# Performance work log

Measured on AMD Instinct MI355X. Metric: run time of the kernel, lower is better.

## Reference

```python
import jax, jax.numpy as jnp
import numpy as np

B, S, H, K, HOP = 32, 512, 768, 4, 3


def setup_inputs() -> dict:
    key = jax.random.key(0)
    ks = jax.random.split(key, 18)
    sc = 0.02
    n = lambda k, shp: (jax.random.normal(k, shp, dtype=jnp.float32) * sc)
    inp = {
        "question": jax.random.normal(ks[0], (B, H), dtype=jnp.float32),
        "text": jax.random.normal(ks[1], (B, S, H), dtype=jnp.float32),
        # per-head MultiheadAttention params (stored as [in,out], i.e. W.T of torch Linear)
        "pw_W": n(ks[2], (K, H, H)), "pw_b": n(ks[3], (K, H)),
        "Ws_W": n(ks[4], (K, H, H)), "Ws_b": n(ks[5], (K, H)),
        "Wt_W": n(ks[6], (K, H, H)), "Wt_b": n(ks[7], (K, H)),
        "We_W": n(ks[8], (K, H)), "We_b": n(ks[9], (K,)),
        # head_weight: Linear(K -> 1)
        "headw_W": n(ks[10], (K,)), "headw_b": n(ks[11], (1,)),
        # GRUCell(input=2H, hidden=H); stored as [in, 3H] (r,z,n order as torch)
        "gru_Wih": n(ks[12], (2 * H, 3 * H)), "gru_Whh": n(ks[13], (H, 3 * H)),
        "gru_bih": n(ks[14], (3 * H,)), "gru_bhh": n(ks[15], (3 * H,)),
        "is_training": 0,
    }
    return inp


def _gru_cell(x, h, Wih, Whh, bih, bhh):
    gx = x @ Wih + bih            # [B,3H]
    gh = h @ Whh + bhh            # [B,3H]
    xr, xz, xn = jnp.split(gx, 3, axis=-1)
    hr, hz, hn = jnp.split(gh, 3, axis=-1)
    r = jax.nn.sigmoid(xr + hr)
    z = jax.nn.sigmoid(xz + hz)
    n = jnp.tanh(xn + r * hn)
    return (1.0 - z) * n + z * h


def reference(question, text, pw_W, pw_b, Ws_W, Ws_b, Wt_W, Wt_b, We_W, We_b,
              headw_W, headw_b, gru_Wih, gru_Whh, gru_bih, gru_bhh, is_training):
    # Dropout layers act as identity (eval mode).
    batch_idx = jnp.arange(text.shape[0])
    # text projection + W_s(text) are question-independent -> hoist out of hop loop
    text_p = jnp.einsum('bsh,khj->kbsj', text, pw_W) + pw_b[:, None, None, :]   # [K,B,S,H]
    W_hs = jnp.einsum('kbsh,khj->kbsj', text_p, Ws_W) + Ws_b[:, None, None, :]  # [K,B,S,H]

    h = jnp.zeros((text.shape[0], H), dtype=question.dtype)
    h_states = []
    predict_prob = None
    for hop in range(HOP):
        W_ht = jnp.einsum('bh,khj->kbj', question, Wt_W) + Wt_b[:, None, :]     # [K,B,H]
        scores = jnp.einsum('kbsh,kh->kbs', jnp.tanh(W_hs + W_ht[:, :, None, :]), We_W) \
                 + We_b[:, None, None]                                          # [K,B,S]
        alpha = jax.nn.softmax(scores, axis=2)                                  # softmax over S
        alpha_linear = jnp.einsum('kbs,k->bs', alpha, headw_W) + headw_b        # [B,S]
        scale = jnp.sqrt(jnp.sum(alpha_linear ** 2, axis=1, keepdims=True))
        prob = alpha_linear / scale
        if hop == 0:
            predict_prob = prob
        idx = jnp.argmax(alpha_linear, axis=1)                                  # [B]
        max_text = text[batch_idx, idx]                                         # [B,H]
        x = jnp.concatenate([question, max_text], axis=1)                       # [B,2H]
        h = _gru_cell(x, h, gru_Wih, gru_Whh, gru_bih, gru_bhh)
        h_states.append(h)
        question = h
    return predict_prob, jnp.stack(h_states, axis=1)                            # [B,S],[B,HOP,H]
```

## Files before the change

kernel.cpp:

```cpp
#include <hip/hip_runtime.h>

typedef unsigned short u16;
typedef __bf16 bf16x8 __attribute__((ext_vector_type(8)));
typedef float f32x4 __attribute__((ext_vector_type(4)));

#define NB 32
#define NS 512
#define NH 768
#define NK 4
#define NBS 16384
#define H3 2304
#define HH 589824

__device__ inline float bf2f(u16 u) {
    unsigned x = ((unsigned)u) << 16;
    return __builtin_bit_cast(float, x);
}
__device__ inline u16 f2bf(float f) {
    unsigned u = __builtin_bit_cast(unsigned, f);
    u += 0x7fffu + ((u >> 16) & 1u);
    return (u16)(u >> 16);
}
__device__ inline float tanh_fast(float x) {
    float e = __expf(2.f * x);
    return 1.f - 2.f * __builtin_amdgcn_rcpf(e + 1.f);
}
__device__ inline float sig_fast(float x) {
    return __builtin_amdgcn_rcpf(1.f + __expf(-x));
}
__device__ inline void gld16(const u16* g, u16* l) {
    __builtin_amdgcn_global_load_lds(
        (const __attribute__((address_space(1))) unsigned int*)g,
        (__attribute__((address_space(3))) unsigned int*)l, 16, 0, 0);
}


__global__ void prep_kernel(const float* __restrict__ WsW, const float* __restrict__ pwb,
                            const float* __restrict__ Wsb, float* __restrict__ combB,
                            const float* __restrict__ question,
                            float* __restrict__ q_f32, float* __restrict__ hT,
                            float* __restrict__ sx, float* __restrict__ sh,
                            const float* __restrict__ Web, float* __restrict__ scores,
                            const float* __restrict__ pwW,
                            u16* __restrict__ WsTH, u16* __restrict__ WsTL,
                            u16* __restrict__ pwH, u16* __restrict__ pwL,
                            const float* __restrict__ text, u16* __restrict__ textH,
                            int tier, int splitText)
{
    int bid = blockIdx.x, t = threadIdx.x;
    if (bid < 48) {
        int idx = bid * 64 + (t >> 2);
        int ph = t & 3;
        int k = idx / NH, j = idx % NH;
        const float* W = WsW + (long)k * HH + j;
        const float* pb = pwb + k * NH;
        float acc = 0.f;
        #pragma unroll 8
        for (int m = ph * 192; m < ph * 192 + 192; ++m)
            acc += pb[m] * W[(long)m * NH];
        acc += __shfl_xor(acc, 1);
        acc += __shfl_xor(acc, 2);
        if (ph == 0) combB[idx] = acc + Wsb[idx];
    } else if (bid < 144) {
        int idx = (bid - 48) * 256 + t;
        q_f32[idx] = question[idx];
    } else if (bid < 240) {
        int idx = (bid - 144) * 256 + t;
        hT[idx] = 0.f;
    } else if (bid < 816) {
        int idx = (bid - 240) * 256 + t;
        if (idx < 73728) sx[idx] = 0.f;
        else sh[idx - 73728] = 0.f;
    } else if (bid < 1072) {
        int idx = (bid - 816) * 256 + t;
        scores[idx] = Web[idx >> 14];
    } else if (bid < 3376) {
        if (tier < 2) return;
        __shared__ float tile[32][33];
        int bid2 = bid - 1072;
        int k = bid2 / 576, rem = bid2 % 576, tr = rem / 24, tc = rem % 24;
        const float* src = WsW + (long)k * HH;
        long dbase = (long)k * HH;
        int tx = t & 31, ty = t >> 5;
        #pragma unroll
        for (int i = 0; i < 4; ++i)
            tile[tx][ty + i*8] = src[(long)(tr*32 + ty + i*8) * NH + tc*32 + tx];
        __syncthreads();
        #pragma unroll
        for (int i = 0; i < 4; ++i) {
            float v = tile[ty + i*8][tx];
            u16 hv = f2bf(v);
            u16 lv = f2bf(v - bf2f(hv));
            long o = dbase + (long)(tc*32 + ty + i*8) * NH + tr*32 + tx;
            WsTH[o] = hv; WsTL[o] = lv;
        }
    } else if (bid < 5680) {
        if (tier < 2) return;
        long base = (long)(bid - 3376) * 1024 + t * 4;
        float4 v = *(const float4*)(pwW + base);
        ushort4 hv, lv;
        hv.x = f2bf(v.x); lv.x = f2bf(v.x - bf2f(hv.x));
        hv.y = f2bf(v.y); lv.y = f2bf(v.y - bf2f(hv.y));
        hv.z = f2bf(v.z); lv.z = f2bf(v.z - bf2f(hv.z));
        hv.w = f2bf(v.w); lv.w = f2bf(v.w - bf2f(hv.w));
        *(ushort4*)(pwH + base) = hv;
        *(ushort4*)(pwL + base) = lv;
    } else {
        if (!splitText) return;
        long base = (long)(bid - 5680) * 1024 + t * 4;
        float4 v = *(const float4*)(text + base);
        ushort4 hv;
        hv.x = f2bf(v.x);
        hv.y = f2bf(v.y);
        hv.z = f2bf(v.z);
        hv.w = f2bf(v.w);
        *(ushort4*)(textH + base) = hv;
    }
}

__global__ __launch_bounds__(256) void comb_mfma_kernel(
    const u16* __restrict__ WsTH, const u16* __restrict__ WsTL,
    const u16* __restrict__ pwH, const u16* __restrict__ pwL,
    u16* __restrict__ combTH, u16* __restrict__ combTL)
{
    __shared__ __align__(16) u16 AsH[128 * 32];
    __shared__ __align__(16) u16 AsL[128 * 32];
    __shared__ __align__(16) u16 BsH[128 * 32];
    __shared__ __align__(16) u16 BsL[128 * 32];
    const int t = threadIdx.x;
    const int wave = t >> 6, lane = t & 63;
    const int k = blockIdx.z;
    const long m0 = (long)blockIdx.x * 128;
    const int n0 = blockIdx.y * 128;
    const u16* AH = WsTH + (long)k * HH;
    const u16* AL = WsTL + (long)k * HH;
    const u16* BH = pwH + (long)k * HH;
    const u16* BL = pwL + (long)k * HH;

    const int r = t >> 2, ch = t & 3;
    const int wm = (wave & 1) * 64, wn = (wave >> 1) * 64;
    const int fr = lane & 15, fq = lane >> 4;

    f32x4 acc[4][4];
    #pragma unroll
    for (int i = 0; i < 4; ++i)
        #pragma unroll
        for (int j = 0; j < 4; ++j) acc[i][j] = (f32x4){0.f, 0.f, 0.f, 0.f};

    for (int k0 = 0; k0 < NH; k0 += 32) {
        gld16(AH + (m0 + r)      * NH + k0 + ch*8, AsH + t*8);
        gld16(AH + (m0 + 64 + r) * NH + k0 + ch*8, AsH + 2048 + t*8);
        gld16(AL + (m0 + r)      * NH + k0 + ch*8, AsL + t*8);
        gld16(AL + (m0 + 64 + r) * NH + k0 + ch*8, AsL + 2048 + t*8);
        gld16(BH + (long)(n0 + r)      * NH + k0 + ch*8, BsH + t*8);
        gld16(BH + (long)(n0 + 64 + r) * NH + k0 + ch*8, BsH + 2048 + t*8);
        gld16(BL + (long)(n0 + r)      * NH + k0 + ch*8, BsL + t*8);
        gld16(BL + (long)(n0 + 64 + r) * NH + k0 + ch*8, BsL + 2048 + t*8);
        __syncthreads();
        bf16x8 afH[4], afL[4], bfH[4], bfL[4];
        #pragma unroll
        for (int i = 0; i < 4; ++i) {
            afH[i] = *(const bf16x8*)(AsH + (wm + i*16 + fr)*32 + fq*8);
            afL[i] = *(const bf16x8*)(AsL + (wm + i*16 + fr)*32 + fq*8);
            bfH[i] = *(const bf16x8*)(BsH + (wn + i*16 + fr)*32 + fq*8);
            bfL[i] = *(const bf16x8*)(BsL + (wn + i*16 + fr)*32 + fq*8);
        }
        #pragma unroll
        for (int i = 0; i < 4; ++i)
            #pragma unroll
            for (int j = 0; j < 4; ++j) {
                acc[i][j] = __builtin_amdgcn_mfma_f32_16x16x32_bf16(afH[i], bfH[j], acc[i][j], 0, 0, 0);
                acc[i][j] = __builtin_amdgcn_mfma_f32_16x16x32_bf16(afH[i], bfL[j], acc[i][j], 0, 0, 0);
                acc[i][j] = __builtin_amdgcn_mfma_f32_16x16x32_bf16(afL[i], bfH[j], acc[i][j], 0, 0, 0);
            }
        __syncthreads();
    }
    long kb = (long)k * HH;
    #pragma unroll
    for (int i = 0; i < 4; ++i) {
        long m = m0 + wm + i*16 + fq*4;
        #pragma unroll
        for (int j = 0; j < 4; ++j) {
            long n = n0 + wn + j*16 + fr;
            #pragma unroll
            for (int rr = 0; rr < 4; ++rr) {
                float v = acc[i][j][rr];
                u16 hv = f2bf(v);
                u16 lv = f2bf(v - bf2f(hv));
                combTH[kb + (m + rr) * NH + n] = hv;
                combTL[kb + (m + rr) * NH + n] = lv;
            }
        }
    }
}

__global__ __launch_bounds__(256) void comb_valu_kernel(
    const float* __restrict__ pwW, const float* __restrict__ WsW,
    float* __restrict__ comb)
{
    __shared__ float AtT[32][68];
    __shared__ float Bt[32][132];
    const int t = threadIdx.x;
    const int m0 = blockIdx.x * 64, j0 = blockIdx.y * 128, k = blockIdx.z;
    const float* A = pwW + (long)k * HH;
    const float* B = WsW + (long)k * HH;
    const int r4 = (t >> 4) * 4, c8 = (t & 15) * 8;
    float acc[4][8];
    #pragma unroll
    for (int rr = 0; rr < 4; ++rr)
        #pragma unroll
        for (int cc = 0; cc < 8; ++cc) acc[rr][cc] = 0.f;
    for (int h0 = 0; h0 < NH; h0 += 32) {
        #pragma unroll
        for (int p = 0; p < 8; ++p) {
            int idx = p * 256 + t;
            int r = idx >> 5, hh = idx & 31;
            AtT[hh][r] = A[(long)(m0 + r) * NH + h0 + hh];
        }
        #pragma unroll
        for (int p = 0; p < 16; ++p) {
            int idx = p * 256 + t;
            int hh = idx >> 7, c = idx & 127;
            Bt[hh][c] = B[(long)(h0 + hh) * NH + j0 + c];
        }
        __syncthreads();
        for (int hh = 0; hh < 32; ++hh) {
            float4 av  = *(const float4*)&AtT[hh][r4];
            float4 bv0 = *(const float4*)&Bt[hh][c8];
            float4 bv1 = *(const float4*)&Bt[hh][c8 + 4];
            float a[4] = {av.x, av.y, av.z, av.w};
            float bb[8] = {bv0.x, bv0.y, bv0.z, bv0.w, bv1.x, bv1.y, bv1.z, bv1.w};
            #pragma unroll
            for (int rr = 0; rr < 4; ++rr)
                #pragma unroll
                for (int cc = 0; cc < 8; ++cc) acc[rr][cc] += a[rr] * bb[cc];
        }
        __syncthreads();
    }
    float* C = comb + (long)k * HH;
    #pragma unroll
    for (int rr = 0; rr < 4; ++rr)
        #pragma unroll
        for (int cc = 0; cc < 8; ++cc)
            C[(long)(m0 + r4 + rr) * NH + j0 + c8 + cc] = acc[rr][cc];
}

__global__ void split_combT_kernel(const float* __restrict__ comb,
                                   u16* __restrict__ combTH, u16* __restrict__ combTL)
{
    __shared__ float tile[32][33];
    int bid = blockIdx.x, t = threadIdx.x;
    int k = bid / 576, rem = bid % 576, tr = rem / 24, tc = rem % 24;
    const float* src = comb + (long)k * HH;
    long dbase = (long)k * HH;
    int tx = t & 31, ty = t >> 5;
    #pragma unroll
    for (int i = 0; i < 4; ++i)
        tile[tx][ty + i*8] = src[(long)(tr*32 + ty + i*8) * NH + tc*32 + tx];
    __syncthreads();
    #pragma unroll
    for (int i = 0; i < 4; ++i) {
        float v = tile[ty + i*8][tx];
        u16 hv = f2bf(v);
        u16 lv = f2bf(v - bf2f(hv));
        long o = dbase + (long)(tc*32 + ty + i*8) * NH + tr*32 + tx;
        combTH[o] = hv; combTL[o] = lv;
    }
}

template <int AM>
__global__ __launch_bounds__(256) void tp_gemm_kernel(
    const float* __restrict__ textf, const u16* __restrict__ textH,
    const u16* __restrict__ combTH, const u16* __restrict__ combTL,
    u16* __restrict__ TP)
{
    __shared__ __align__(16) u16 AsH[128 * 64];
    __shared__ __align__(16) u16 BsH[128 * 64];
    __shared__ __align__(16) u16 BsL[128 * 64];
    const int t = threadIdx.x;
    const int wave = t >> 6, lane = t & 63;
    const int k = blockIdx.z;
    const long m0 = (long)blockIdx.x * 128;
    const int n0 = blockIdx.y * 128;
    const u16* BH = combTH + (long)k * HH;
    const u16* BL = combTL + (long)k * HH;

    const int r = t >> 3, ch = t & 7;
    const int wm = (wave & 1) * 64, wn = (wave >> 1) * 64;
    const int fr = lane & 15, fq = lane >> 4;

    f32x4 acc[4][4];
    #pragma unroll
    for (int i = 0; i < 4; ++i)
        #pragma unroll
        for (int j = 0; j < 4; ++j) acc[i][j] = (f32x4){0.f, 0.f, 0.f, 0.f};

    for (int h0 = 0; h0 < NH; h0 += 64) {
        if (AM) {
            #pragma unroll
            for (int q = 0; q < 4; ++q)
                gld16(textH + (m0 + q*32 + r) * NH + h0 + ch*8, AsH + q*2048 + t*8);
        } else {
            #pragma unroll
            for (int p = 0; p < 8; ++p) {
                int task = p * 256 + t;
                int row = task >> 4, g = task & 15;
                float4 v = *(const float4*)(textf + (m0 + row) * NH + h0 + g*4);
                ushort4 hv;
                hv.x = f2bf(v.x);
                hv.y = f2bf(v.y);
                hv.z = f2bf(v.z);
                hv.w = f2bf(v.w);
                *(ushort4*)(AsH + row * 64 + g*4) = hv;
            }
        }
        #pragma unroll
        for (int q = 0; q < 4; ++q) {
            gld16(BH + (long)(n0 + q*32 + r) * NH + h0 + ch*8, BsH + q*2048 + t*8);
            gld16(BL + (long)(n0 + q*32 + r) * NH + h0 + ch*8, BsL + q*2048 + t*8);
        }
        __syncthreads();
        #pragma unroll
        for (int ks = 0; ks < 2; ++ks) {
            bf16x8 afH[4], bfH[4], bfL[4];
            #pragma unroll
            for (int i = 0; i < 4; ++i) {
                afH[i] = *(const bf16x8*)(AsH + (wm + i*16 + fr)*64 + ks*32 + fq*8);
                bfH[i] = *(const bf16x8*)(BsH + (wn + i*16 + fr)*64 + ks*32 + fq*8);
                bfL[i] = *(const bf16x8*)(BsL + (wn + i*16 + fr)*64 + ks*32 + fq*8);
            }
            #pragma unroll
            for (int i = 0; i < 4; ++i)
                #pragma unroll
                for (int j = 0; j < 4; ++j) {
                    acc[i][j] = __builtin_amdgcn_mfma_f32_16x16x32_bf16(afH[i], bfH[j], acc[i][j], 0, 0, 0);
                    acc[i][j] = __builtin_amdgcn_mfma_f32_16x16x32_bf16(afH[i], bfL[j], acc[i][j], 0, 0, 0);
                }
        }
        __syncthreads();
    }
    u16* out = TP + ((long)k * NBS + m0) * NH + n0;
    #pragma unroll
    for (int i = 0; i < 4; ++i) {
        #pragma unroll
        for (int rr = 0; rr < 4; ++rr) {
            int m = wm + i*16 + fq*4 + rr;
            #pragma unroll
            for (int j = 0; j < 4; ++j) {
                int n = wn + j*16 + fr;
                out[(long)m * NH + n] = f2bf(acc[i][j][rr]);
            }
        }
    }
}

__global__ __launch_bounds__(256) void score_pass_kernel(
    const u16* __restrict__ TP, const float* __restrict__ W_ht,
    const float* __restrict__ WeW, const float* __restrict__ Web,
    float* __restrict__ scores)
{
    __shared__ __align__(16) float bias_s[NH];
    __shared__ __align__(16) float we_s[NH];
    const int t = threadIdx.x;
    const int k = blockIdx.z, b = blockIdx.y;
    const int s0 = blockIdx.x * 32;
    for (int i = t; i < NH; i += 256) {
        bias_s[i] = W_ht[((k << 5) + b) * NH + i];
        we_s[i]   = WeW[k * NH + i];
    }
    __syncthreads();
    const int wave = t >> 6, lane = t & 63;
    const u16* tpb = TP + ((long)k * NBS + (b << 9) + s0) * NH;
    const float web = Web[k];
    for (int sr = wave; sr < 32; sr += 4) {
        const u16* row = tpb + (long)sr * NH;
        float part = 0.f;
        #pragma unroll
        for (int p = 0; p < 3; ++p) {
            const int j = p * 256 + lane * 4;
            ushort4 v = *(const ushort4*)(row + j);
            float4 bb = *(const float4*)(bias_s + j);
            float4 ww = *(const float4*)(we_s + j);
            part += tanh_fast(bf2f(v.x) + bb.x) * ww.x;
            part += tanh_fast(bf2f(v.y) + bb.y) * ww.y;
            part += tanh_fast(bf2f(v.z) + bb.z) * ww.z;
            part += tanh_fast(bf2f(v.w) + bb.w) * ww.w;
        }
        part += __shfl_xor(part, 1);
        part += __shfl_xor(part, 2);
        part += __shfl_xor(part, 4);
        part += __shfl_xor(part, 8);
        part += __shfl_xor(part, 16);
        part += __shfl_xor(part, 32);
        if (lane == 0) scores[(((k << 5) + b) << 9) + s0 + sr] = part + web;
    }
}

__global__ void init_scores_kernel(const float* __restrict__ Web,
                                   float* __restrict__ scores, int koff)
{
    int idx = (koff << 14) + blockIdx.x * 256 + threadIdx.x;
    scores[idx] = Web[idx >> 14];
}

__global__ __launch_bounds__(256) void wht2_kernel(
    const float* __restrict__ q, const float* __restrict__ WtW,
    const float* __restrict__ combB, const float* __restrict__ Wtb,
    float* __restrict__ W_ht)
{
    int bid = blockIdx.x;
    int k = bid / 96, rem = bid % 96, b = rem / 3, jt = rem % 3;
    int j = jt * 256 + threadIdx.x;
    const float* W = WtW + (long)k * HH + j;
    const float* qb = q + b * NH;
    float acc = 0.f;
    #pragma unroll 8
    for (int h = 0; h < NH; ++h) acc += qb[h] * W[(long)h * NH];
    W_ht[(k*NB + b) * NH + j] = acc + Wtb[k * NH + j] + combB[k * NH + j];
}

template <int AM>
__global__ __launch_bounds__(256) void fused_scores_mfma(
    const float* __restrict__ textf,
    const u16* __restrict__ textH, const u16* __restrict__ textL,
    const u16* __restrict__ combTH, const u16* __restrict__ combTL,
    const float* __restrict__ W_ht,
    const float* __restrict__ WeW, float* __restrict__ scores, int koff)
{
    __shared__ __align__(16) u16 AsH[128 * 32];
    __shared__ __align__(16) u16 AsL[128 * 32];
    __shared__ __align__(16) u16 BsH[128 * 32];
    __shared__ __align__(16) u16 BsL[128 * 32];
    __shared__ float wht_s[128];
    __shared__ float we_s[128];
    __shared__ float sred[128];
    const int t = threadIdx.x;
    const int wave = t >> 6, lane = t & 63;
    const int k = koff + blockIdx.z;
    const long m0 = (long)blockIdx.x * 128;
    const int n0 = blockIdx.y * 128;
    const int b = (int)(m0 >> 9), srow = (int)(m0 & 511);
    const u16* BH = combTH + (long)k * HH;
    const u16* BL = combTL + (long)k * HH;

    if (t < 128) {
        wht_s[t] = W_ht[((k << 5) + b) * NH + n0 + t];
        we_s[t]  = WeW[k * NH + n0 + t];
        sred[t]  = 0.f;
    }

    const int r = t >> 2, ch = t & 3;
    const int wm = (wave & 1) * 64, wn = (wave >> 1) * 64;
    const int fr = lane & 15, fq = lane >> 4;

    f32x4 acc[4][4];
    #pragma unroll
    for (int i = 0; i < 4; ++i)
        #pragma unroll
        for (int j = 0; j < 4; ++j) acc[i][j] = (f32x4){0.f, 0.f, 0.f, 0.f};

    for (int h0 = 0; h0 < NH; h0 += 32) {
        if (AM) {
            gld16(textH + (m0 + r)      * NH + h0 + ch*8, AsH + t*8);
            gld16(textH + (m0 + 64 + r) * NH + h0 + ch*8, AsH + 2048 + t*8);
            gld16(textL + (m0 + r)      * NH + h0 + ch*8, AsL + t*8);
            gld16(textL + (m0 + 64 + r) * NH + h0 + ch*8, AsL + 2048 + t*8);
        } else {
            #pragma unroll
            for (int p = 0; p < 4; ++p) {
                int task = p * 256 + t;
                int row = task >> 3, g = task & 7;
                float4 v = *(const float4*)(textf + (m0 + row) * NH + h0 + g*4);
                ushort4 hv, lv;
                hv.x = f2bf(v.x); lv.x = f2bf(v.x - bf2f(hv.x));
                hv.y = f2bf(v.y); lv.y = f2bf(v.y - bf2f(hv.y));
                hv.z = f2bf(v.z); lv.z = f2bf(v.z - bf2f(hv.z));
                hv.w = f2bf(v.w); lv.w = f2bf(v.w - bf2f(hv.w));
                *(ushort4*)(AsH + row * 32 + g*4) = hv;
                *(ushort4*)(AsL + row * 32 + g*4) = lv;
            }
        }
        gld16(BH + (long)(n0 + r)      * NH + h0 + ch*8, BsH + t*8);
        gld16(BH + (long)(n0 + 64 + r) * NH + h0 + ch*8, BsH + 2048 + t*8);
        gld16(BL + (long)(n0 + r)      * NH + h0 + ch*8, BsL + t*8);
        gld16(BL + (long)(n0 + 64 + r) * NH + h0 + ch*8, BsL + 2048 + t*8);
        __syncthreads();
        bf16x8 afH[4], afL[4], bfH[4], bfL[4];
        #pragma unroll
        for (int i = 0; i < 4; ++i) {
            afH[i] = *(const bf16x8*)(AsH + (wm + i*16 + fr)*32 + fq*8);
            afL[i] = *(const bf16x8*)(AsL + (wm + i*16 + fr)*32 + fq*8);
            bfH[i] = *(const bf16x8*)(BsH + (wn + i*16 + fr)*32 + fq*8);
            bfL[i] = *(const bf16x8*)(BsL + (wn + i*16 + fr)*32 + fq*8);
        }
        #pragma unroll
        for (int i = 0; i < 4; ++i)
            #pragma unroll
            for (int j = 0; j < 4; ++j) {
                acc[i][j] = __builtin_amdgcn_mfma_f32_16x16x32_bf16(afH[i], bfH[j], acc[i][j], 0, 0, 0);
                acc[i][j] = __builtin_amdgcn_mfma_f32_16x16x32_bf16(afH[i], bfL[j], acc[i][j], 0, 0, 0);
                acc[i][j] = __builtin_amdgcn_mfma_f32_16x16x32_bf16(afL[i], bfH[j], acc[i][j], 0, 0, 0);
            }
        __syncthreads();
    }
    #pragma unroll
    for (int i = 0; i < 4; ++i) {
        #pragma unroll
        for (int rr = 0; rr < 4; ++rr) {
            int m = wm + i*16 + fq*4 + rr;
            float part = 0.f;
            #pragma unroll
            for (int j = 0; j < 4; ++j) {
                int n = wn + j*16 + fr;
                part += tanh_fast(acc[i][j][rr] + wht_s[n]) * we_s[n];
            }
            part += __shfl_xor(part, 1);
            part += __shfl_xor(part, 2);
            part += __shfl_xor(part, 4);
            part += __shfl_xor(part, 8);
            if (fr == 0) atomicAdd(&sred[m], part);
        }
    }
    __syncthreads();
    if (t < 128)
        atomicAdd(&scores[(((k << 5) + b) << 9) + srow + t], sred[t]);
}

__global__ __launch_bounds__(256) void fused_scores_valu(
    const float* __restrict__ text, const float* __restrict__ comb,
    const float* __restrict__ W_ht,
    const float* __restrict__ WeW, float* __restrict__ scores)
{
    __shared__ float AtT[32][68];
    __shared__ float Bt[32][132];
    __shared__ float wht_s[128];
    __shared__ float we_s[128];
    __shared__ float sred[64];
    const int t = threadIdx.x;
    const int row0 = blockIdx.x * 64;
    const int j0 = blockIdx.y * 128, k = blockIdx.z;
    const int b = row0 >> 9, s0 = row0 & 511;
    const float* B = comb + (long)k * HH;
    const int r4 = (t >> 4) * 4, c8 = (t & 15) * 8;
    if (t < 128) {
        wht_s[t] = W_ht[((k << 5) + b) * NH + j0 + t];
        we_s[t]  = WeW[k * NH + j0 + t];
    }
    if (t < 64) sred[t] = 0.f;
    float acc[4][8];
    #pragma unroll
    for (int rr = 0; rr < 4; ++rr)
        #pragma unroll
        for (int cc = 0; cc < 8; ++cc) acc[rr][cc] = 0.f;
    for (int h0 = 0; h0 < NH; h0 += 32) {
        #pragma unroll
        for (int p = 0; p < 8; ++p) {
            int idx = p * 256 + t;
            int r = idx >> 5, hh = idx & 31;
            AtT[hh][r] = text[(long)(row0 + r) * NH + h0 + hh];
        }
        #pragma unroll
        for (int p = 0; p < 16; ++p) {
            int idx = p * 256 + t;
            int hh = idx >> 7, c = idx & 127;
            Bt[hh][c] = B[(long)(h0 + hh) * NH + j0 + c];
        }
        __syncthreads();
        for (int hh = 0; hh < 32; ++hh) {
            float4 av  = *(const float4*)&AtT[hh][r4];
            float4 bv0 = *(const float4*)&Bt[hh][c8];
            float4 bv1 = *(const float4*)&Bt[hh][c8 + 4];
            float a[4] = {av.x, av.y, av.z, av.w};
            float bb[8] = {bv0.x, bv0.y, bv0.z, bv0.w, bv1.x, bv1.y, bv1.z, bv1.w};
            #pragma unroll
            for (int rr = 0; rr < 4; ++rr)
                #pragma unroll
                for (int cc = 0; cc < 8; ++cc) acc[rr][cc] += a[rr] * bb[cc];
        }
        __syncthreads();
    }
    float part[4] = {0.f, 0.f, 0.f, 0.f};
    #pragma unroll
    for (int rr = 0; rr < 4; ++rr)
        #pragma unroll
        for (int cc = 0; cc < 8; ++cc)
            part[rr] += tanh_fast(acc[rr][cc] + wht_s[c8 + cc]) * we_s[c8 + cc];
    #pragma unroll
    for (int rr = 0; rr < 4; ++rr)
        atomicAdd(&sred[r4 + rr], part[rr]);
    __syncthreads();
    if (t < 64)
        atomicAdd(&scores[(((k << 5) + b) << 9) + s0 + t], sred[t]);
}

__global__ void softmax_kernel(const float* __restrict__ scores,
                               const float* __restrict__ headw_W, const float* __restrict__ headw_b,
                               const float* __restrict__ text,
                               const float* __restrict__ q_f32,
                               float* __restrict__ xT, float* __restrict__ out_prob, int hop)
{
    __shared__ float sc[NK][NS];
    __shared__ float cred[4];
    __shared__ float cval[4];
    __shared__ int   cidx[4];
    int b = blockIdx.x, t = threadIdx.x;
    int wave = t >> 6, lane = t & 63;
    for (int i = t; i < NK * NS; i += 256) {
        int k = i >> 9, s = i & 511;
        sc[k][s] = scores[((k*NB + b) << 9) + s];
    }
    __syncthreads();
    float fac[NK];
    for (int k = 0; k < NK; ++k) {
        float v0 = sc[k][t], v1 = sc[k][t + 256];
        float m = fmaxf(v0, v1);
        #pragma unroll
        for (int o = 32; o > 0; o >>= 1) m = fmaxf(m, __shfl_xor(m, o));
        if (lane == 0) cred[wave] = m;
        __syncthreads();
        float mx = fmaxf(fmaxf(cred[0], cred[1]), fmaxf(cred[2], cred[3]));
        __syncthreads();
        float e0 = __expf(v0 - mx), e1 = __expf(v1 - mx);
        sc[k][t] = e0; sc[k][t + 256] = e1;
        float sm = e0 + e1;
        #pragma unroll
        for (int o = 32; o > 0; o >>= 1) sm += __shfl_xor(sm, o);
        if (lane == 0) cred[wave] = sm;
        __syncthreads();
        fac[k] = headw_W[k] / (cred[0] + cred[1] + cred[2] + cred[3]);
        __syncthreads();
    }
    float hwb = headw_b[0];
    float a0 = hwb, a1 = hwb;
    for (int k = 0; k < NK; ++k) { a0 += sc[k][t] * fac[k]; a1 += sc[k][t + 256] * fac[k]; }
    float ss = a0*a0 + a1*a1;
    #pragma unroll
    for (int o = 32; o > 0; o >>= 1) ss += __shfl_xor(ss, o);
    float bv; int bi;
    if (a0 >= a1) { bv = a0; bi = t; } else { bv = a1; bi = t + 256; }
    #pragma unroll
    for (int o = 1; o < 64; o <<= 1) {
        float ov = __shfl_xor(bv, o);
        int   oi = __shfl_xor(bi, o);
        if (ov > bv || (ov == bv && oi < bi)) { bv = ov; bi = oi; }
    }
    if (lane == 0) { cred[wave] = ss; cval[wave] = bv; cidx[wave] = bi; }
    __syncthreads();
    float scale = sqrtf(cred[0] + cred[1] + cred[2] + cred[3]);
    float mbv = cval[0]; int mbi = cidx[0];
    #pragma unroll
    for (int w = 1; w < 4; ++w)
        if (cval[w] > mbv || (cval[w] == mbv && cidx[w] < mbi)) { mbv = cval[w]; mbi = cidx[w]; }
    int idx = mbi;
    if (hop == 0) {
        out_prob[(b << 9) + t]       = a0 / scale;
        out_prob[(b << 9) + t + 256] = a1 / scale;
    }
    const float* trow = text + (long)(b * NS + idx) * NH;
    for (int i = t; i < NH; i += 256) {
        xT[i * NB + b]        = q_f32[b*NH + i];
        xT[(NH + i) * NB + b] = trow[i];
    }
}

__global__ __launch_bounds__(256) void gru_mm3_kernel(
    const float* __restrict__ Wih, const float* __restrict__ Whh,
    const float* __restrict__ xT, const float* __restrict__ hT,
    float* __restrict__ sx, float* __restrict__ sh)
{
    __shared__ float xs[8192];
    int t = threadIdx.x;
    int tj = t & 63, tq = t >> 6;
    int j = blockIdx.x * 64 + tj;
    int cg = blockIdx.y;
    const float* W; const float* src; float* dst; int c;
    if (cg < 6) { W = Wih; src = xT; dst = sx; c = cg; }
    else        { W = Whh; src = hT; dst = sh; c = cg - 6; }
    for (int idx = t; idx < 8192; idx += 256) xs[idx] = src[c * 8192 + idx];
    __syncthreads();
    float acc[8];
    #pragma unroll
    for (int bq = 0; bq < 8; ++bq) acc[bq] = 0.f;
    #pragma unroll 8
    for (int ii = 0; ii < 256; ++ii) {
        float w = W[(long)(c * 256 + ii) * H3 + j];
        #pragma unroll
        for (int bq = 0; bq < 8; ++bq) acc[bq] += xs[ii * 32 + tq * 8 + bq] * w;
    }
    #pragma unroll
    for (int bq = 0; bq < 8; ++bq)
        atomicAdd(&dst[(long)(tq * 8 + bq) * H3 + j], acc[bq]);
}

__global__ void gate_kernel(const float* __restrict__ bih, const float* __restrict__ bhh,
                            float* __restrict__ sx, float* __restrict__ sh,
                            float* __restrict__ hT, float* __restrict__ q_f32,
                            float* __restrict__ out_h, int hop)
{
    int gid = blockIdx.x * 256 + threadIdx.x;
    int b = gid / NH, j = gid % NH;
    float xr = bih[j]        + sx[b*H3 + j];
    float xz = bih[NH + j]   + sx[b*H3 + NH + j];
    float xn = bih[1536 + j] + sx[b*H3 + 1536 + j];
    float hr = bhh[j]        + sh[b*H3 + j];
    float hz = bhh[NH + j]   + sh[b*H3 + NH + j];
    float hn = bhh[1536 + j] + sh[b*H3 + 1536 + j];
    sx[b*H3 + j] = 0.f; sx[b*H3 + NH + j] = 0.f; sx[b*H3 + 1536 + j] = 0.f;
    sh[b*H3 + j] = 0.f; sh[b*H3 + NH + j] = 0.f; sh[b*H3 + 1536 + j] = 0.f;
    float r = sig_fast(xr + hr);
    float z = sig_fast(xz + hz);
    float n = tanh_fast(xn + r * hn);
    float hp = hT[j * NB + b];
    float hnew = (1.f - z) * n + z * hp;
    hT[j * NB + b] = hnew;
    q_f32[gid] = hnew;
    out_h[(long)(b * 3 + hop) * NH + j] = hnew;
}

extern "C" void kernel_launch(void* const* d_in, const int* in_sizes, int n_in,
                              void* d_out, int out_size, void* d_ws, size_t ws_size,
                              hipStream_t stream)
{
    const float* question = (const float*)d_in[0];
    const float* text     = (const float*)d_in[1];
    const float* pw_W     = (const float*)d_in[2];
    const float* pw_b     = (const float*)d_in[3];
    const float* Ws_W     = (const float*)d_in[4];
    const float* Ws_b     = (const float*)d_in[5];
    const float* Wt_W     = (const float*)d_in[6];
    const float* Wt_b     = (const float*)d_in[7];
    const float* We_W     = (const float*)d_in[8];
    const float* We_b     = (const float*)d_in[9];
    const float* headw_W  = (const float*)d_in[10];
    const float* headw_b  = (const float*)d_in[11];
    const float* Wih      = (const float*)d_in[12];
    const float* Whh      = (const float*)d_in[13];
    const float* bih      = (const float*)d_in[14];
    const float* bhh      = (const float*)d_in[15];

    char* ws = (char*)d_ws;
    float* comb   = (float*)(ws + 0);
    float* combB  = (float*)(ws + 9437184);
    float* W_ht   = (float*)(ws + 9449472);
    float* scores = (float*)(ws + 9842688);
    float* q_f32  = (float*)(ws + 10104832);
    float* hT     = (float*)(ws + 10203136);
    float* xT     = (float*)(ws + 10301440);
    float* sx     = (float*)(ws + 10498048);
    float* sh     = (float*)(ws + 10792960);
    u16*   combTH = (u16*)  (ws + 11087872);
    u16*   combTL = (u16*)  (ws + 15806464);
    u16*   TP     = (u16*)  (ws + 20525056);
    u16*   textH  = (u16*)  (ws + 121188352);
    u16*   WsTH   = (u16*)  (ws + 20525056);
    u16*   WsTL   = (u16*)  (ws + 25243648);
    u16*   pwH    = (u16*)  (ws + 29962240);
    u16*   pwL    = (u16*)  (ws + 34680832);

    int nstore = 0;
    if (ws_size >= (size_t)70856704) {
        long avail = (long)ws_size - 20525056L;
        nstore = (int)(avail / 25165824L);
        if (nstore > NK) nstore = NK;
    }
    const int tier = (nstore >= 1) ? 3
                   : (ws_size >= (size_t)20525056) ? 1 : 0;
    const bool haveTextH = (tier == 3) && (nstore == NK)
                        && (ws_size >= (size_t)146354176);

    float* out_prob = (float*)d_out;
    float* out_h    = (float*)d_out + NB * NS;

    const int prepGrid = haveTextH ? 17968 : (tier >= 2 ? 5680 : 1072);
    prep_kernel<<<prepGrid, 256, 0, stream>>>(
        Ws_W, pw_b, Ws_b, combB, question, q_f32, hT, sx, sh, We_b, scores,
        pw_W, WsTH, WsTL, pwH, pwL, text, textH,
        tier >= 3 ? 2 : tier, haveTextH ? 1 : 0);

    if (tier == 3) {
        comb_mfma_kernel<<<dim3(6, 6, 4), 256, 0, stream>>>(WsTH, WsTL, pwH, pwL,
                                                            combTH, combTL);
        if (haveTextH) {
            tp_gemm_kernel<1><<<dim3(128, 6, nstore), 256, 0, stream>>>(
                text, textH, combTH, combTL, TP);
        } else {
            tp_gemm_kernel<0><<<dim3(128, 6, nstore), 256, 0, stream>>>(
                text, nullptr, combTH, combTL, TP);
        }
    } else {
        comb_valu_kernel<<<dim3(12, 6, 4), 256, 0, stream>>>(pw_W, Ws_W, comb);
        if (tier == 1)
            split_combT_kernel<<<2304, 256, 0, stream>>>(comb, combTH, combTL);
    }

    for (int hop = 0; hop < 3; ++hop) {
        wht2_kernel<<<384, 256, 0, stream>>>(q_f32, Wt_W, combB, Wt_b, W_ht);
        if (tier == 3) {
            score_pass_kernel<<<dim3(16, 32, nstore), 256, 0, stream>>>(
                TP, W_ht, We_W, We_b, scores);
            if (nstore < NK) {
                if (hop > 0)
                    init_scores_kernel<<<(NK - nstore) * 64, 256, 0, stream>>>(
                        We_b, scores, nstore);
                fused_scores_mfma<0><<<dim3(128, 6, NK - nstore), 256, 0, stream>>>(
                    text, nullptr, nullptr, combTH, combTL, W_ht, We_W,
                    scores, nstore);
            }
        } else if (tier == 1) {
            init_scores_kernel<<<256, 256, 0, stream>>>(We_b, scores, 0);
            fused_scores_mfma<0><<<dim3(128, 6, 4), 256, 0, stream>>>(
                text, nullptr, nullptr, combTH, combTL, W_ht, We_W, scores, 0);
        } else {
            init_scores_kernel<<<256, 256, 0, stream>>>(We_b, scores, 0);
            fused_scores_valu<<<dim3(256, 6, 4), 256, 0, stream>>>(
                text, comb, W_ht, We_W, scores);
        }
        softmax_kernel<<<32, 256, 0, stream>>>(scores, headw_W, headw_b, text,
                                               q_f32, xT, out_prob, hop);
        gru_mm3_kernel<<<dim3(36, 9), 256, 0, stream>>>(Wih, Whh, xT, hT, sx, sh);
        gate_kernel<<<96, 256, 0, stream>>>(bih, bhh, sx, sh, hT, q_f32, out_h, hop);
    }
}
```

Baseline: 630.7 us.

## Fuse hop loop into one persistent cooperative kernel with grid syncs

Replaces the per-hop sequence of separate launches (W_ht projection, score pass, softmax/argmax, GRU matmul, gate) with a single cooperative kernel of 1024 blocks that runs all three hops, separating stages with grid-wide synchronisation. It targets launch overhead and inter-kernel gaps, which matter because several stages use only a handful of blocks. In exchange, every stage runs on a fixed grid with many idle blocks, grid.sync has its own cost, and the fused kernel needs enough occupancy for 1024 co-resident blocks. If the cooperative launch fails, the old multi-kernel path runs instead.

```diff
diff --git a/kernel.cpp b/kernel.cpp
--- a/kernel.cpp
+++ b/kernel.cpp
@@ -1,4 +1,7 @@
 #include <hip/hip_runtime.h>
+#include <hip/hip_cooperative_groups.h>
+
+namespace cg = cooperative_groups;
 
 typedef unsigned short u16;
 typedef __bf16 bf16x8 __attribute__((ext_vector_type(8)));
@@ -354,6 +357,186 @@
     }
 }
 
+__global__ __launch_bounds__(256, 4) void hop_loop_kernel(
+    const u16* __restrict__ TP, float* __restrict__ W_ht,
+    const float* __restrict__ combB,
+    const float* __restrict__ WtW, const float* __restrict__ Wtb,
+    const float* __restrict__ WeW, const float* __restrict__ Web,
+    float* __restrict__ scores,
+    const float* __restrict__ headw_W, const float* __restrict__ headw_b,
+    const float* __restrict__ text,
+    float* __restrict__ q_f32, float* __restrict__ hT, float* __restrict__ xT,
+    float* __restrict__ sx, float* __restrict__ sh,
+    const float* __restrict__ Wih, const float* __restrict__ Whh,
+    const float* __restrict__ bih, const float* __restrict__ bhh,
+    float* __restrict__ out_prob, float* __restrict__ out_h)
+{
+    cg::grid_group grid = cg::this_grid();
+    __shared__ __align__(16) float smem[8192];
+    __shared__ float cred[4];
+    __shared__ float cval[4];
+    __shared__ int   cidx[4];
+    const int bid = blockIdx.x, t = threadIdx.x;
+    const int wave = t >> 6, lane = t & 63;
+
+    for (int hop = 0; hop < 3; ++hop) {
+        if (bid < 384) {
+            int k = bid / 96, rem = bid % 96, b = rem / 3, jt = rem % 3;
+            int j = jt * 256 + t;
+            const float* W = WtW + (long)k * HH + j;
+            const float* qb = q_f32 + b * NH;
+            float acc = 0.f;
+            #pragma unroll 8
+            for (int h = 0; h < NH; ++h) acc += qb[h] * W[(long)h * NH];
+            W_ht[(k*NB + b) * NH + j] = acc + Wtb[k * NH + j] + combB[k * NH + j];
+        }
+        grid.sync();
+        {
+            int k = bid >> 8, rem = bid & 255;
+            int b = rem >> 3, chunk = rem & 7;
+            int s0 = chunk * 64;
+            float* bias_s = smem;
+            float* we_s   = smem + 768;
+            for (int i = t; i < NH; i += 256) {
+                bias_s[i] = W_ht[((k << 5) + b) * NH + i];
+                we_s[i]   = WeW[k * NH + i];
+            }
+            __syncthreads();
+            const u16* tpb = TP + ((long)k * NBS + (b << 9) + s0) * NH;
+            const float web = Web[k];
+            for (int sr = wave; sr < 64; sr += 4) {
+                const u16* row = tpb + (long)sr * NH;
+                float part = 0.f;
+                #pragma unroll
+                for (int p = 0; p < 3; ++p) {
+                    const int j = p * 256 + lane * 4;
+                    ushort4 v = *(const ushort4*)(row + j);
+                    float4 bb = *(const float4*)(bias_s + j);
+                    float4 ww = *(const float4*)(we_s + j);
+                    part += tanh_fast(bf2f(v.x) + bb.x) * ww.x;
+                    part += tanh_fast(bf2f(v.y) + bb.y) * ww.y;
+                    part += tanh_fast(bf2f(v.z) + bb.z) * ww.z;
+                    part += tanh_fast(bf2f(v.w) + bb.w) * ww.w;
+                }
+                part += __shfl_xor(part, 1);
+                part += __shfl_xor(part, 2);
+                part += __shfl_xor(part, 4);
+                part += __shfl_xor(part, 8);
+                part += __shfl_xor(part, 16);
+                part += __shfl_xor(part, 32);
+                if (lane == 0) scores[(((k << 5) + b) << 9) + s0 + sr] = part + web;
+            }
+        }
+        grid.sync();
+        if (bid < NB) {
+            int b = bid;
+            float (*sc)[NS] = (float(*)[NS])smem;
+            for (int i = t; i < NK * NS; i += 256) {
+                int k = i >> 9, s = i & 511;
+                sc[k][s] = scores[((k*NB + b) << 9) + s];
+            }
+            __syncthreads();
+            float fac[NK];
+            for (int k = 0; k < NK; ++k) {
+                float v0 = sc[k][t], v1 = sc[k][t + 256];
+                float m = fmaxf(v0, v1);
+                #pragma unroll
+                for (int o = 32; o > 0; o >>= 1) m = fmaxf(m, __shfl_xor(m, o));
+                if (lane == 0) cred[wave] = m;
+                __syncthreads();
+                float mx = fmaxf(fmaxf(cred[0], cred[1]), fmaxf(cred[2], cred[3]));
+                __syncthreads();
+                float e0 = __expf(v0 - mx), e1 = __expf(v1 - mx);
+                sc[k][t] = e0; sc[k][t + 256] = e1;
+                float sm = e0 + e1;
+                #pragma unroll
+                for (int o = 32; o > 0; o >>= 1) sm += __shfl_xor(sm, o);
+                if (lane == 0) cred[wave] = sm;
+                __syncthreads();
+                fac[k] = headw_W[k] / (cred[0] + cred[1] + cred[2] + cred[3]);
+                __syncthreads();
+            }
+            float hwb = headw_b[0];
+            float a0 = hwb, a1 = hwb;
+            for (int k = 0; k < NK; ++k) { a0 += sc[k][t] * fac[k]; a1 += sc[k][t + 256] * fac[k]; }
+            float ss = a0*a0 + a1*a1;
+            #pragma unroll
+            for (int o = 32; o > 0; o >>= 1) ss += __shfl_xor(ss, o);
+            float bv; int bi;
+            if (a0 >= a1) { bv = a0; bi = t; } else { bv = a1; bi = t + 256; }
+            #pragma unroll
+            for (int o = 1; o < 64; o <<= 1) {
+                float ov = __shfl_xor(bv, o);
+                int   oi = __shfl_xor(bi, o);
+                if (ov > bv || (ov == bv && oi < bi)) { bv = ov; bi = oi; }
+            }
+            if (lane == 0) { cred[wave] = ss; cval[wave] = bv; cidx[wave] = bi; }
+            __syncthreads();
+            float scale = sqrtf(cred[0] + cred[1] + cred[2] + cred[3]);
+            float mbv = cval[0]; int mbi = cidx[0];
+            #pragma unroll
+            for (int w = 1; w < 4; ++w)
+                if (cval[w] > mbv || (cval[w] == mbv && cidx[w] < mbi)) { mbv = cval[w]; mbi = cidx[w]; }
+            int idx = mbi;
+            if (hop == 0) {
+                out_prob[(b << 9) + t]       = a0 / scale;
+                out_prob[(b << 9) + t + 256] = a1 / scale;
+            }
+            const float* trow = text + (long)(b * NS + idx) * NH;
+            for (int i = t; i < NH; i += 256) {
+                xT[i * NB + b]        = q_f32[b*NH + i];
+                xT[(NH + i) * NB + b] = trow[i];
+            }
+        }
+        grid.sync();
+        if (bid < 324) {
+            float* xs = smem;
+            int jx = bid % 36, cgi = bid / 36;
+            int tj = t & 63, tq = t >> 6;
+            int j = jx * 64 + tj;
+            const float* W; const float* src; float* dst; int c;
+            if (cgi < 6) { W = Wih; src = xT; dst = sx; c = cgi; }
+            else         { W = Whh; src = hT; dst = sh; c = cgi - 6; }
+            for (int idx = t; idx < 8192; idx += 256) xs[idx] = src[c * 8192 + idx];
+            __syncthreads();
+            float acc[8];
+            #pragma unroll
+            for (int bq = 0; bq < 8; ++bq) acc[bq] = 0.f;
+            #pragma unroll 8
+            for (int ii = 0; ii < 256; ++ii) {
+                float w = W[(long)(c * 256 + ii) * H3 + j];
+                #pragma unroll
+                for (int bq = 0; bq < 8; ++bq) acc[bq] += xs[ii * 32 + tq * 8 + bq] * w;
+            }
+            #pragma unroll
+            for (int bq = 0; bq < 8; ++bq)
+                atomicAdd(&dst[(long)(tq * 8 + bq) * H3 + j], acc[bq]);
+        }
+        grid.sync();
+        if (bid < 96) {
+            int gid = bid * 256 + t;
+            int b = gid / NH, j = gid % NH;
+            float xr = bih[j]        + sx[b*H3 + j];
+            float xz = bih[NH + j]   + sx[b*H3 + NH + j];
+            float xn = bih[1536 + j] + sx[b*H3 + 1536 + j];
+            float hr = bhh[j]        + sh[b*H3 + j];
+            float hz = bhh[NH + j]   + sh[b*H3 + NH + j];
+            float hn = bhh[1536 + j] + sh[b*H3 + 1536 + j];
+            sx[b*H3 + j] = 0.f; sx[b*H3 + NH + j] = 0.f; sx[b*H3 + 1536 + j] = 0.f;
+            sh[b*H3 + j] = 0.f; sh[b*H3 + NH + j] = 0.f; sh[b*H3 + 1536 + j] = 0.f;
+            float r = sig_fast(xr + hr);
+            float z = sig_fast(xz + hz);
+            float n = tanh_fast(xn + r * hn);
+            float hp = hT[j * NB + b];
+            float hnew = (1.f - z) * n + z * hp;
+            hT[j * NB + b] = hnew;
+            q_f32[gid] = hnew;
+            out_h[(long)(b * 3 + hop) * NH + j] = hnew;
+        }
+        grid.sync();
+    }
+}
+
 __global__ __launch_bounds__(256) void score_pass_kernel(
     const u16* __restrict__ TP, const float* __restrict__ W_ht,
     const float* __restrict__ WeW, const float* __restrict__ Web,
@@ -672,10 +855,10 @@
     int t = threadIdx.x;
     int tj = t & 63, tq = t >> 6;
     int j = blockIdx.x * 64 + tj;
-    int cg = blockIdx.y;
+    int cgi = blockIdx.y;
     const float* W; const float* src; float* dst; int c;
-    if (cg < 6) { W = Wih; src = xT; dst = sx; c = cg; }
-    else        { W = Whh; src = hT; dst = sh; c = cg - 6; }
+    if (cgi < 6) { W = Wih; src = xT; dst = sx; c = cgi; }
+    else         { W = Whh; src = hT; dst = sh; c = cgi - 6; }
     for (int idx = t; idx < 8192; idx += 256) xs[idx] = src[c * 8192 + idx];
     __syncthreads();
     float acc[8];
@@ -793,31 +976,50 @@
             split_combT_kernel<<<2304, 256, 0, stream>>>(comb, combTH, combTL);
     }
 
-    for (int hop = 0; hop < 3; ++hop) {
-        wht2_kernel<<<384, 256, 0, stream>>>(q_f32, Wt_W, combB, Wt_b, W_ht);
-        if (tier == 3) {
-            score_pass_kernel<<<dim3(16, 32, nstore), 256, 0, stream>>>(
-                TP, W_ht, We_W, We_b, scores);
-            if (nstore < NK) {
-                if (hop > 0)
-                    init_scores_kernel<<<(NK - nstore) * 64, 256, 0, stream>>>(
-                        We_b, scores, nstore);
-                fused_scores_mfma<0><<<dim3(128, 6, NK - nstore), 256, 0, stream>>>(
-                    text, nullptr, nullptr, combTH, combTL, W_ht, We_W,
-                    scores, nstore);
-            }
-        } else if (tier == 1) {
-            init_scores_kernel<<<256, 256, 0, stream>>>(We_b, scores, 0);
-            fused_scores_mfma<0><<<dim3(128, 6, 4), 256, 0, stream>>>(
-                text, nullptr, nullptr, combTH, combTL, W_ht, We_W, scores, 0);
-        } else {
-            init_scores_kernel<<<256, 256, 0, stream>>>(We_b, scores, 0);
-            fused_scores_valu<<<dim3(256, 6, 4), 256, 0, stream>>>(
-                text, comb, W_ht, We_W, scores);
-        }
-        softmax_kernel<<<32, 256, 0, stream>>>(scores, headw_W, headw_b, text,
-                                               q_f32, xT, out_prob, hop);
-        gru_mm3_kernel<<<dim3(36, 9), 256, 0, stream>>>(Wih, Whh, xT, hT, sx, sh);
-        gate_kernel<<<96, 256, 0, stream>>>(bih, bhh, sx, sh, hT, q_f32, out_h, hop);
-    }
-}
+    bool coopDone = false;
+    if (tier == 3 && nstore == NK) {
+        void* args[] = {
+            (void*)&TP, (void*)&W_ht, (void*)&combB, (void*)&Wt_W, (void*)&Wt_b,
+            (void*)&We_W, (void*)&We_b, (void*)&scores,
+            (void*)&headw_W, (void*)&headw_b, (void*)&text,
+            (void*)&q_f32, (void*)&hT, (void*)&xT, (void*)&sx, (void*)&sh,
+            (void*)&Wih, (void*)&Whh, (void*)&bih, (void*)&bhh,
+            (void*)&out_prob, (void*)&out_h
+        };
+        hipError_t cerr = hipLaunchCooperativeKernel(
+            reinterpret_cast<void*>(hop_loop_kernel),
+            dim3(1024), dim3(256), args, 0, stream);
+        if (cerr == hipSuccess) coopDone = true;
+        else (void)hipGetLastError();
+    }
+
+    if (!coopDone) {
+        for (int hop = 0; hop < 3; ++hop) {
+            wht2_kernel<<<384, 256, 0, stream>>>(q_f32, Wt_W, combB, Wt_b, W_ht);
+            if (tier == 3) {
+                score_pass_kernel<<<dim3(16, 32, nstore), 256, 0, stream>>>(
+                    TP, W_ht, We_W, We_b, scores);
+                if (nstore < NK) {
+                    if (hop > 0)
+                        init_scores_kernel<<<(NK - nstore) * 64, 256, 0, stream>>>(
+                            We_b, scores, nstore);
+                    fused_scores_mfma<0><<<dim3(128, 6, NK - nstore), 256, 0, stream>>>(
+                        text, nullptr, nullptr, combTH, combTL, W_ht, We_W,
+                        scores, nstore);
+                }
+            } else if (tier == 1) {
+                init_scores_kernel<<<256, 256, 0, stream>>>(We_b, scores, 0);
+                fused_scores_mfma<0><<<dim3(128, 6, 4), 256, 0, stream>>>(
+                    text, nullptr, nullptr, combTH, combTL, W_ht, We_W, scores, 0);
+            } else {
+                init_scores_kernel<<<256, 256, 0, stream>>>(We_b, scores, 0);
+                fused_scores_valu<<<dim3(256, 6, 4), 256, 0, stream>>>(
+                    text, comb, W_ht, We_W, scores);
+            }
+            softmax_kernel<<<32, 256, 0, stream>>>(scores, headw_W, headw_b, text,
+                                                   q_f32, xT, out_prob, hop);
+            gru_mm3_kernel<<<dim3(36, 9), 256, 0, stream>>>(Wih, Whh, xT, hT, sx, sh);
+            gate_kernel<<<96, 256, 0, stream>>>(bih, bhh, sx, sh, hT, q_f32, out_h, hop);
+        }
+    }
+}
```

Result: slower. 2.445 ms (+287.7%).
